# Performance work log

Hardware: AMD Instinct MI355X
Metric: run time of the kernel (lower is better)

Reference implementation:

```python
import math
import jax, jax.numpy as jnp
import numpy as np

B, N, L, D = 4, 16, 1024, 64  # batch, heads, seq len (L1=L2), head dim


def rel_shift(x):
    """Transformer-XL positional shift: [b,n,q,p]->[b,n,q,k] aligning relative positions."""
    b, n, q, k = x.shape
    x = jnp.pad(x, ((0, 0), (0, 0), (0, 0), (1, 0)))  # pad one zero column in front
    x = x.reshape(b, n, k + 1, q)
    return x[:, :, 1:, :].reshape(b, n, q, k)


def setup_inputs() -> dict:
    rng = jax.random.key(0)
    k1, k2, k3, k4, k5 = jax.random.split(rng, 5)
    query_content_biased = jax.random.normal(k1, (B, N, L, D), dtype=jnp.float32)
    query_pos_biased = jax.random.normal(k2, (B, N, L, D), dtype=jnp.float32)
    key = jax.random.normal(k3, (B, N, L, D), dtype=jnp.float32)
    value = jax.random.normal(k4, (B, N, L, D), dtype=jnp.float32)
    pos_encodings = jax.random.normal(k5, (N, L, D), dtype=jnp.float32)
    # causal mask: True = masked (as in torch masked_fill), broadcast over b,n
    mask = jnp.triu(jnp.ones((L, L), dtype=bool), k=1)[None, None]
    return {
        "query_content_biased": query_content_biased,
        "query_pos_biased": query_pos_biased,
        "key": key,
        "value": value,
        "pos_encodings": pos_encodings,
        "mask": mask,
    }


def reference(query_content_biased, query_pos_biased, key, value, pos_encodings, mask):
    # content scores: [b,n,i,j]
    weight = jnp.einsum('bnid,bnjd->bnij', query_content_biased, key)
    # positional scores, shifted into key axis
    pos_scores = jnp.einsum('bnid,npd->bnip', query_pos_biased, pos_encodings)
    weight = weight + rel_shift(pos_scores)
    weight = weight / math.sqrt(key.shape[-1])
    neg = jnp.finfo(weight.dtype).min
    weight = jnp.where(mask, neg, weight)
    weight = jax.nn.softmax(weight, axis=-1)
    weight = jnp.where(mask, jnp.zeros((), weight.dtype), weight)
    # dropout is identity at p=0.0 (eval)
    out = jnp.einsum('bnij,bnjd->bnid', weight, value)
    return (out, weight)
```

## Files before the change

kernel.cpp:

```cpp
#include <hip/hip_runtime.h>
#include <math.h>


#define Bq 4
#define Nh 16
#define Lq 1024
#define Dh 64
#define TQ 16
#define NT 512
#define LROW 1032

#define BAR() asm volatile("s_waitcnt lgkmcnt(0)\n\ts_barrier" ::: "memory")

typedef _Float16 h16;
typedef __attribute__((ext_vector_type(8))) _Float16 f16x8;
typedef __attribute__((ext_vector_type(4))) _Float16 f16x4;
typedef __attribute__((ext_vector_type(4))) float f32x4;

__device__ __forceinline__ f16x8 pack8h(float4 a, float4 b) {
    f16x8 o;
    o[0] = (h16)a.x; o[1] = (h16)a.y; o[2] = (h16)a.z; o[3] = (h16)a.w;
    o[4] = (h16)b.x; o[5] = (h16)b.y; o[6] = (h16)b.z; o[7] = (h16)b.w;
    return o;
}

__device__ __forceinline__ float wave_max(float v) {
    #pragma unroll
    for (int o = 32; o > 0; o >>= 1) v = fmaxf(v, __shfl_xor(v, o));
    return v;
}
__device__ __forceinline__ float wave_sum(float v) {
    #pragma unroll
    for (int o = 32; o > 0; o >>= 1) v += __shfl_xor(v, o);
    return v;
}

__global__ __launch_bounds__(256) void cvt_kp_kernel(
    const float* __restrict__ K, const float* __restrict__ P,
    h16* __restrict__ Kb, h16* __restrict__ Pb)
{
    int b = blockIdx.x;
    const float* src; h16* dst; int idx;
    if (b < 4096) { idx = b * 256 + threadIdx.x; src = K; dst = Kb; }
    else          { idx = (b - 4096) * 256 + threadIdx.x; src = P; dst = Pb; }
    float4 v = ((const float4*)src)[idx];
    f16x4 o;
    o[0] = (h16)v.x; o[1] = (h16)v.y; o[2] = (h16)v.z; o[3] = (h16)v.w;
    ((f16x4*)dst)[idx] = o;
}

__global__ __launch_bounds__(256) void vt_kernel(
    const float* __restrict__ V, h16* __restrict__ Vt)
{
    __shared__ float t[64][65];
    int bn = blockIdx.x >> 4, jt = blockIdx.x & 15;
    int tid = threadIdx.x;
    int d = tid & 63, q = tid >> 6;
    const float* vb = V + ((size_t)(bn * Lq + jt * 64)) * Dh;
    #pragma unroll
    for (int r = 0; r < 16; r++) {
        int jl = r * 4 + q;
        t[jl][d] = vb[(size_t)jl * Dh + d];
    }
    __syncthreads();
    int dd = tid >> 2, jb = (tid & 3) << 4;
    f16x8 s0, s1;
    #pragma unroll
    for (int jj = 0; jj < 8; jj++) {
        s0[jj] = (h16)t[jb + jj][dd];
        s1[jj] = (h16)t[jb + 8 + jj][dd];
    }
    h16* drow = Vt + (((size_t)(bn * 64 + dd)) << 10) + (jt << 6) + jb;
    *(f16x8*)drow = s0;
    *(f16x8*)(drow + 8) = s1;
}

__global__ __launch_bounds__(NT, 8) void relattn_kernel(
    const float* __restrict__ QC, const float* __restrict__ QP,
    const h16* __restrict__ Kb, const h16* __restrict__ Pb,
    const h16* __restrict__ Vtb,
    float* __restrict__ out, float* __restrict__ wout)
{
    __shared__ __align__(16) h16 s_s[TQ][LROW];
    __shared__ __align__(16) float dscr[4][64][4];

    const int tid  = threadIdx.x;
    const int w    = tid >> 6, lane = tid & 63;
    const int ln   = lane & 15, quad = lane >> 4;

    const int bidx = blockIdx.x;
    const int wg   = ((bidx & 7) << 9) | (bidx >> 3);
    const int bn   = wg >> 6, qt = 63 - (wg & 63);
    const int nh   = bn & 15;
    const int i0   = qt << 4, i1 = i0 + 15;

    const float* qcrow = QC + (((size_t)(bn << 10) + i0 + ln) << 6) + (quad << 3);
    const float* qprow = QP + (((size_t)(bn << 10) + i0 + ln) << 6) + (quad << 3);
    f16x8 aC0 = pack8h(*(const float4*)qcrow,        *(const float4*)(qcrow + 4));
    f16x8 aC1 = pack8h(*(const float4*)(qcrow + 32), *(const float4*)(qcrow + 36));
    f16x8 aP0 = pack8h(*(const float4*)qprow,        *(const float4*)(qprow + 4));
    f16x8 aP1 = pack8h(*(const float4*)(qprow + 32), *(const float4*)(qprow + 36));

    const h16* kbase = Kb + (((size_t)(bn << 10)) << 6) + (quad << 3);
    #pragma unroll
    for (int ct = 0; ct < 8; ct++) {
        int c0 = ((ct << 3) + w) << 4;
        if (c0 <= i1) {
            const h16* kr = kbase + ((size_t)(c0 + ln) << 6);
            f32x4 acc = {0.f, 0.f, 0.f, 0.f};
            acc = __builtin_amdgcn_mfma_f32_16x16x32_f16(aC0, *(const f16x8*)kr,        acc, 0, 0, 0);
            acc = __builtin_amdgcn_mfma_f32_16x16x32_f16(aC1, *(const f16x8*)(kr + 32), acc, 0, 0, 0);
            #pragma unroll
            for (int rg = 0; rg < 4; rg++)
                s_s[(quad << 2) + rg][c0 + ln] = (h16)acc[rg];
        }
    }
    BAR();

    const h16* pbase = Pb + (((size_t)(nh << 10)) << 6) + (quad << 3);
    #pragma unroll
    for (int ct = 0; ct < 8; ct++) {
        int p0 = ((ct << 3) + w) << 4;
        if (p0 + i0 + 30 >= 1023) {
            const h16* pr = pbase + ((size_t)(p0 + ln) << 6);
            f32x4 acc = {0.f, 0.f, 0.f, 0.f};
            acc = __builtin_amdgcn_mfma_f32_16x16x32_f16(aP0, *(const f16x8*)pr,        acc, 0, 0, 0);
            acc = __builtin_amdgcn_mfma_f32_16x16x32_f16(aP1, *(const f16x8*)(pr + 32), acc, 0, 0, 0);
            int p = p0 + ln;
            #pragma unroll
            for (int rg = 0; rg < 4; rg++) {
                int row = (quad << 2) + rg;
                int j = p + i0 + row - 1023;
                if (j >= 0)
                    s_s[row][j] = (h16)((float)s_s[row][j] + acc[rg]);
            }
        }
    }
    BAR();

    #pragma unroll
    for (int rr = 0; rr < 2; rr++) {
        int r = (w << 1) + rr;
        int i = i0 + r;
        float v[16];
        #pragma unroll
        for (int c = 0; c < 4; c++) {
            f16x4 t = *(f16x4*)&s_s[r][(c << 8) + (lane << 2)];
            v[c * 4 + 0] = (float)t[0]; v[c * 4 + 1] = (float)t[1];
            v[c * 4 + 2] = (float)t[2]; v[c * 4 + 3] = (float)t[3];
        }
        float mx = -3.0e38f;
        #pragma unroll
        for (int c = 0; c < 4; c++) {
            int j = (c << 8) + (lane << 2);
            #pragma unroll
            for (int e = 0; e < 4; e++)
                if (j + e <= i) mx = fmaxf(mx, v[c * 4 + e]);
        }
        mx = wave_max(mx);
        float sum = 0.f;
        #pragma unroll
        for (int c = 0; c < 4; c++) {
            int j = (c << 8) + (lane << 2);
            #pragma unroll
            for (int e = 0; e < 4; e++) {
                float t = (j + e <= i) ? __expf((v[c * 4 + e] - mx) * 0.125f) : 0.f;
                sum += t;
                v[c * 4 + e] = t;
            }
        }
        sum = wave_sum(sum);
        float inv = 1.0f / sum;
        float* wrow = wout + (((size_t)(bn << 10) + i) << 10);
        #pragma unroll
        for (int c = 0; c < 4; c++) {
            int j = (c << 8) + (lane << 2);
            float4 e;
            e.x = v[c * 4 + 0] * inv; e.y = v[c * 4 + 1] * inv;
            e.z = v[c * 4 + 2] * inv; e.w = v[c * 4 + 3] * inv;
            *(float4*)&wrow[j] = e;
            f16x4 hh;
            hh[0] = (h16)e.x; hh[1] = (h16)e.y; hh[2] = (h16)e.z; hh[3] = (h16)e.w;
            *(f16x4*)&s_s[r][j] = hh;
        }
    }
    BAR();

    f32x4 o = {0.f, 0.f, 0.f, 0.f};
    const int n0 = (w & 3) << 4;
    const int h  = w >> 2;
    const h16* vtb = Vtb + (((size_t)(bn << 6) + n0 + ln) << 10);
    const h16* abase = &s_s[ln][0];
    const int ksteps = (i0 + 16 + 31) >> 5;
    for (int ks = h; ks < ksteps; ks += 2) {
        int k0 = (ks << 5) + (quad << 3);
        f16x8 af = *(const f16x8*)(abase + k0);
        f16x8 vb = *(const f16x8*)(vtb + k0);
        o = __builtin_amdgcn_mfma_f32_16x16x32_f16(af, vb, o, 0, 0, 0);
    }
    if (h == 1)
        *(f32x4*)&dscr[w & 3][lane][0] = o;
    BAR();
    if (h == 0) {
        f32x4 o2 = *(f32x4*)&dscr[w][lane][0];
        o[0] += o2[0]; o[1] += o2[1]; o[2] += o2[2]; o[3] += o2[3];
        float* obase = out + (((size_t)(bn << 10) + i0) << 6);
        #pragma unroll
        for (int rg = 0; rg < 4; rg++)
            obase[((size_t)((quad << 2) + rg) << 6) + n0 + ln] = o[rg];
    }
}

extern "C" void kernel_launch(void* const* d_in, const int* in_sizes, int n_in,
                              void* d_out, int out_size, void* d_ws, size_t ws_size,
                              hipStream_t stream) {
    const float* qc = (const float*)d_in[0];
    const float* qp = (const float*)d_in[1];
    const float* K  = (const float*)d_in[2];
    const float* V  = (const float*)d_in[3];
    const float* P  = (const float*)d_in[4];

    float* out  = (float*)d_out;
    float* wout = out + (size_t)Bq * Nh * Lq * Dh;

    const size_t NQ = (size_t)Bq * Nh * Lq * Dh;
    const size_t NP = (size_t)Nh * Lq * Dh;
    h16* Kb  = (h16*)d_ws;
    h16* Pb  = Kb + NQ;
    h16* Vtb = Pb + NP;

    cvt_kp_kernel<<<4096 + 1024, 256, 0, stream>>>(K, P, Kb, Pb);
    vt_kernel<<<Bq * Nh * 16, 256, 0, stream>>>(V, Vtb);
    relattn_kernel<<<Bq * Nh * (Lq / TQ), NT, 0, stream>>>(qc, qp, Kb, Pb, Vtb, out, wout);
}
```

Before: 441.6 us.

## Merge prep kernels, pre-mask scores with -inf, and use nontemporal output stores

Merges the K/P fp16 conversion and the V transpose into one prep launch, which removes one kernel launch and its gap. The main kernel now writes -inf into masked score positions in shared memory, so the softmax drops its per-element causal compares and can use a fast reciprocal. The weight and output writes become nontemporal stores to reduce cache pollution. The -inf fill adds shared-memory writes, and the rcp approximation slightly changes rounding.

```diff
diff --git a/kernel.cpp b/kernel.cpp
--- a/kernel.cpp
+++ b/kernel.cpp
@@ -35,25 +35,25 @@
     return v;
 }
 
-__global__ __launch_bounds__(256) void cvt_kp_kernel(
+__global__ __launch_bounds__(256) void prep_kernel(
     const float* __restrict__ K, const float* __restrict__ P,
-    h16* __restrict__ Kb, h16* __restrict__ Pb)
-{
-    int b = blockIdx.x;
-    const float* src; h16* dst; int idx;
-    if (b < 4096) { idx = b * 256 + threadIdx.x; src = K; dst = Kb; }
-    else          { idx = (b - 4096) * 256 + threadIdx.x; src = P; dst = Pb; }
-    float4 v = ((const float4*)src)[idx];
-    f16x4 o;
-    o[0] = (h16)v.x; o[1] = (h16)v.y; o[2] = (h16)v.z; o[3] = (h16)v.w;
-    ((f16x4*)dst)[idx] = o;
-}
-
-__global__ __launch_bounds__(256) void vt_kernel(
-    const float* __restrict__ V, h16* __restrict__ Vt)
+    const float* __restrict__ V,
+    h16* __restrict__ Kb, h16* __restrict__ Pb, h16* __restrict__ Vt)
 {
     __shared__ float t[64][65];
-    int bn = blockIdx.x >> 4, jt = blockIdx.x & 15;
+    int b = blockIdx.x;
+    if (b < 5120) {
+        const float* src; h16* dst; int idx;
+        if (b < 4096) { idx = b * 256 + threadIdx.x; src = K; dst = Kb; }
+        else          { idx = (b - 4096) * 256 + threadIdx.x; src = P; dst = Pb; }
+        float4 v = ((const float4*)src)[idx];
+        f16x4 o;
+        o[0] = (h16)v.x; o[1] = (h16)v.y; o[2] = (h16)v.z; o[3] = (h16)v.w;
+        ((f16x4*)dst)[idx] = o;
+        return;
+    }
+    int bv = b - 5120;
+    int bn = bv >> 4, jt = bv & 15;
     int tid = threadIdx.x;
     int d = tid & 63, q = tid >> 6;
     const float* vb = V + ((size_t)(bn * Lq + jt * 64)) * Dh;
@@ -101,6 +101,20 @@
     f16x8 aP0 = pack8h(*(const float4*)qprow,        *(const float4*)(qprow + 4));
     f16x8 aP1 = pack8h(*(const float4*)(qprow + 32), *(const float4*)(qprow + 36));
 
+    {
+        f16x8 nf;
+        #pragma unroll
+        for (int k = 0; k < 8; k++) nf[k] = (h16)-INFINITY;
+        int rr0 = tid >> 7;
+        int tt  = tid & 127;
+        int col = i0 + 16 + (tt << 3);
+        if (col < 1024) {
+            #pragma unroll
+            for (int r = rr0; r < 16; r += 4)
+                *(f16x8*)&s_s[r][col] = nf;
+        }
+    }
+
     const h16* kbase = Kb + (((size_t)(bn << 10)) << 6) + (quad << 3);
     #pragma unroll
     for (int ct = 0; ct < 8; ct++) {
@@ -111,8 +125,11 @@
             acc = __builtin_amdgcn_mfma_f32_16x16x32_f16(aC0, *(const f16x8*)kr,        acc, 0, 0, 0);
             acc = __builtin_amdgcn_mfma_f32_16x16x32_f16(aC1, *(const f16x8*)(kr + 32), acc, 0, 0, 0);
             #pragma unroll
-            for (int rg = 0; rg < 4; rg++)
-                s_s[(quad << 2) + rg][c0 + ln] = (h16)acc[rg];
+            for (int rg = 0; rg < 4; rg++) {
+                int row = (quad << 2) + rg;
+                float val = (c0 + ln <= i0 + row) ? acc[rg] : -INFINITY;
+                s_s[row][c0 + ln] = (h16)val;
+            }
         }
     }
     BAR();
@@ -149,38 +166,29 @@
             v[c * 4 + 0] = (float)t[0]; v[c * 4 + 1] = (float)t[1];
             v[c * 4 + 2] = (float)t[2]; v[c * 4 + 3] = (float)t[3];
         }
-        float mx = -3.0e38f;
+        float mx = v[0];
+        #pragma unroll
+        for (int k = 1; k < 16; k++) mx = fmaxf(mx, v[k]);
+        mx = wave_max(mx);
+        float sum = 0.f;
+        #pragma unroll
+        for (int k = 0; k < 16; k++) {
+            float t = __expf((v[k] - mx) * 0.125f);
+            sum += t;
+            v[k] = t;
+        }
+        sum = wave_sum(sum);
+        float inv = __builtin_amdgcn_rcpf(sum);
+        float* wrow = wout + (((size_t)(bn << 10) + i) << 10);
         #pragma unroll
         for (int c = 0; c < 4; c++) {
             int j = (c << 8) + (lane << 2);
-            #pragma unroll
-            for (int e = 0; e < 4; e++)
-                if (j + e <= i) mx = fmaxf(mx, v[c * 4 + e]);
-        }
-        mx = wave_max(mx);
-        float sum = 0.f;
-        #pragma unroll
-        for (int c = 0; c < 4; c++) {
-            int j = (c << 8) + (lane << 2);
-            #pragma unroll
-            for (int e = 0; e < 4; e++) {
-                float t = (j + e <= i) ? __expf((v[c * 4 + e] - mx) * 0.125f) : 0.f;
-                sum += t;
-                v[c * 4 + e] = t;
-            }
-        }
-        sum = wave_sum(sum);
-        float inv = 1.0f / sum;
-        float* wrow = wout + (((size_t)(bn << 10) + i) << 10);
-        #pragma unroll
-        for (int c = 0; c < 4; c++) {
-            int j = (c << 8) + (lane << 2);
-            float4 e;
-            e.x = v[c * 4 + 0] * inv; e.y = v[c * 4 + 1] * inv;
-            e.z = v[c * 4 + 2] * inv; e.w = v[c * 4 + 3] * inv;
-            *(float4*)&wrow[j] = e;
+            f32x4 e;
+            e[0] = v[c * 4 + 0] * inv; e[1] = v[c * 4 + 1] * inv;
+            e[2] = v[c * 4 + 2] * inv; e[3] = v[c * 4 + 3] * inv;
+            __builtin_nontemporal_store(e, (f32x4*)&wrow[j]);
             f16x4 hh;
-            hh[0] = (h16)e.x; hh[1] = (h16)e.y; hh[2] = (h16)e.z; hh[3] = (h16)e.w;
+            hh[0] = (h16)e[0]; hh[1] = (h16)e[1]; hh[2] = (h16)e[2]; hh[3] = (h16)e[3];
             *(f16x4*)&s_s[r][j] = hh;
         }
     }
@@ -207,7 +215,8 @@
         float* obase = out + (((size_t)(bn << 10) + i0) << 6);
         #pragma unroll
         for (int rg = 0; rg < 4; rg++)
-            obase[((size_t)((quad << 2) + rg) << 6) + n0 + ln] = o[rg];
+            __builtin_nontemporal_store(
+                o[rg], &obase[((size_t)((quad << 2) + rg) << 6) + n0 + ln]);
     }
 }
 
@@ -229,7 +238,6 @@
     h16* Pb  = Kb + NQ;
     h16* Vtb = Pb + NP;
 
-    cvt_kp_kernel<<<4096 + 1024, 256, 0, stream>>>(K, P, Kb, Pb);
-    vt_kernel<<<Bq * Nh * 16, 256, 0, stream>>>(V, Vtb);
+    prep_kernel<<<4096 + 1024 + 1024, 256, 0, stream>>>(K, P, V, Kb, Pb, Vtb);
     relattn_kernel<<<Bq * Nh * (Lq / TQ), NT, 0, stream>>>(qc, qp, Kb, Pb, Vtb, out, wout);
 }
```

Measured after the change: 432.5 us. 2.1% less time.
